# Performance work log

Hardware: AMD Instinct MI355X
Metric: run time of the kernel (lower is better)

Reference implementation:

```python
import jax, jax.numpy as jnp
import numpy as np

D_MODEL = 1024
N = 32  # d_state // 2
L_LEN = 4096


def setup_inputs() -> dict:
    key = jax.random.key(0)
    k1, k2, k3 = jax.random.split(key, 3)
    dt_min, dt_max = 1e-3, 1e-1
    log_dt = jax.random.uniform(k1, (D_MODEL,), dtype=jnp.float32) * (
        np.log(dt_max) - np.log(dt_min)
    ) + np.log(dt_min)
    C_ri = jax.random.normal(k2, (D_MODEL, N, 2), dtype=jnp.float32)
    log_A_real = jnp.log(0.5 * jnp.ones((D_MODEL, N), dtype=jnp.float32))
    A_imag = np.pi * jnp.broadcast_to(
        jnp.arange(N, dtype=jnp.float32)[None, :], (D_MODEL, N)
    )
    return {
        "L": L_LEN,
        "log_dt": log_dt,
        "C_ri": C_ri,
        "log_A_real": log_A_real,
        "A_imag": A_imag,
    }


def reference(L, log_dt, C_ri, log_A_real, A_imag):
    dt = jnp.exp(log_dt)  # (H,)
    C = C_ri[..., 0] + 1j * C_ri[..., 1]  # (H, N) complex
    A = -jnp.exp(log_A_real) + 1j * A_imag  # (H, N)
    dtA = A * dt[:, None]  # (H, N)
    # Vandermonde: exp(dtA * l) for l in [0, L)
    l = jnp.arange(L, dtype=jnp.float32)
    V = jnp.exp(dtA[:, :, None] * l[None, None, :])  # (H, N, L) complex
    Ceff = C * (jnp.exp(dtA) - 1.0) / A  # (H, N)
    K = 2.0 * jnp.einsum("hn,hnl->hl", Ceff, V).real  # (H, L)
    return K
```

## Files before the change

kernel.cpp:

```cpp
#include <hip/hip_runtime.h>


#define HD   1024
#define NS   32
#define LL   4096
#define BLK  256
#define NJ   (LL / BLK)

__global__ __launch_bounds__(BLK) void s4d_kernel(
    const float* __restrict__ log_dt,
    const float* __restrict__ C_ri,
    const float* __restrict__ log_A_real,
    const float* __restrict__ A_imag,
    float* __restrict__ K)
{
    const int h   = blockIdx.x;
    const int tid = threadIdx.x;

    __shared__ float  s_wr[NS], s_wi[NS];
    __shared__ float  s_cr[NS], s_ci[NS];
    __shared__ float  s_a[NS];
    __shared__ double s_b[NS];

    const double TWO_PI     = 6.283185307179586;
    const double INV_TWO_PI = 0.15915494309189535;

    if (tid < NS) {
        const int   n   = tid;
        const float dt  = expf(log_dt[h]);
        const float ar  = -expf(log_A_real[h * NS + n]);
        const float ai  = A_imag[h * NS + n];
        const float a   = ar * dt;
        const double bd = (double)ai * (double)dt;
        const float b   = (float)bd;

        const float e = expf(a);
        float sb, cb;
        sincosf(b, &sb, &cb);
        const float er = fmaf(e, cb, -1.0f);
        const float ei = e * sb;

        const float den = fmaf(ar, ar, ai * ai);
        const float inv = 1.0f / den;
        const float fr  = fmaf(er, ar,  ei * ai) * inv;
        const float fi  = fmaf(ei, ar, -er * ai) * inv;

        const float Cr = C_ri[(h * NS + n) * 2 + 0];
        const float Ci = C_ri[(h * NS + n) * 2 + 1];
        s_cr[n] = 2.0f * fmaf(Cr, fr, -Ci * fi);
        s_ci[n] = 2.0f * fmaf(Cr, fi,  Ci * fr);

        double ph = bd * 256.0;
        ph -= floor(ph * INV_TWO_PI) * TWO_PI;
        float sw, cw;
        sincosf((float)ph, &sw, &cw);
        const float e256 = expf(a * 256.0f);
        s_wr[n] = e256 * cw;
        s_wi[n] = e256 * sw;
        s_a[n]  = a;
        s_b[n]  = bd;
    }
    __syncthreads();

    float acc[NJ];
#pragma unroll
    for (int j = 0; j < NJ; ++j) acc[j] = 0.0f;

    for (int n = 0; n < NS; ++n) {
        const float  a = s_a[n];
        const double b = s_b[n];

        const float mag = expf(a * (float)tid);
        double ph = b * (double)tid;
        ph -= floor(ph * INV_TWO_PI) * TWO_PI;
        float sp, cp;
        sincosf((float)ph, &sp, &cp);
        float zr = mag * cp;
        float zi = mag * sp;

        const float wr = s_wr[n], wi = s_wi[n];
        const float cr = s_cr[n], ci = s_ci[n];

#pragma unroll
        for (int j = 0; j < NJ; ++j) {
            acc[j] = fmaf(cr, zr, fmaf(-ci, zi, acc[j]));
            const float t = fmaf(zr, wr, -zi * wi);
            zi = fmaf(zr, wi, zi * wr);
            zr = t;
        }
    }

    float* out = K + h * LL + tid;
#pragma unroll
    for (int j = 0; j < NJ; ++j) out[j * BLK] = acc[j];
}

extern "C" void kernel_launch(void* const* d_in, const int* in_sizes, int n_in,
                              void* d_out, int out_size, void* d_ws, size_t ws_size,
                              hipStream_t stream) {
    const float* log_dt     = (const float*)d_in[1];
    const float* C_ri       = (const float*)d_in[2];
    const float* log_A_real = (const float*)d_in[3];
    const float* A_imag     = (const float*)d_in[4];
    float* K = (float*)d_out;

    s4d_kernel<<<dim3(HD), dim3(BLK), 0, stream>>>(log_dt, C_ri, log_A_real, A_imag, K);
}
```

Baseline: 94.10 us.

## Use a real second-order recurrence with packed float2 math over paired modes

```diff
diff --git a/kernel.cpp b/kernel.cpp
--- a/kernel.cpp
+++ b/kernel.cpp
@@ -6,6 +6,8 @@
 #define LL   4096
 #define BLK  256
 #define NJ   (LL / BLK)
+
+typedef float v2 __attribute__((ext_vector_type(2)));
 
 __global__ __launch_bounds__(BLK) void s4d_kernel(
     const float* __restrict__ log_dt,
@@ -17,16 +19,19 @@
     const int h   = blockIdx.x;
     const int tid = threadIdx.x;
 
-    __shared__ float  s_wr[NS], s_wi[NS];
-    __shared__ float  s_cr[NS], s_ci[NS];
-    __shared__ float  s_a[NS];
-    __shared__ double s_b[NS];
+    __shared__ v2 s_wr[NS / 2], s_wi[NS / 2];
+    __shared__ v2 s_q[NS / 2];
+    __shared__ v2 s_c2r[NS / 2], s_c2i[NS / 2];
+    __shared__ v2 s_al2[NS / 2];
+    __shared__ double s_rb[NS];
 
     const double TWO_PI     = 6.283185307179586;
     const double INV_TWO_PI = 0.15915494309189535;
+    const float  TWO_PI_F   = 6.2831853f;
 
     if (tid < NS) {
         const int   n   = tid;
+        const int   sl  = ((n & 15) << 1) | (n >> 4);
         const float dt  = expf(log_dt[h]);
         const float ar  = -expf(log_A_real[h * NS + n]);
         const float ai  = A_imag[h * NS + n];
@@ -47,52 +52,71 @@
 
         const float Cr = C_ri[(h * NS + n) * 2 + 0];
         const float Ci = C_ri[(h * NS + n) * 2 + 1];
-        s_cr[n] = 2.0f * fmaf(Cr, fr, -Ci * fi);
-        s_ci[n] = 2.0f * fmaf(Cr, fi,  Ci * fr);
+        ((float*)s_c2r)[sl] = 2.0f * fmaf(Cr, fr, -Ci * fi);
+        ((float*)s_c2i)[sl] = 2.0f * fmaf(Cr, fi,  Ci * fr);
 
         double ph = bd * 256.0;
         ph -= floor(ph * INV_TWO_PI) * TWO_PI;
         float sw, cw;
         sincosf((float)ph, &sw, &cw);
         const float e256 = expf(a * 256.0f);
-        s_wr[n] = e256 * cw;
-        s_wi[n] = e256 * sw;
-        s_a[n]  = a;
-        s_b[n]  = bd;
+        ((float*)s_wr)[sl]  = e256 * cw;
+        ((float*)s_wi)[sl]  = e256 * sw;
+        ((float*)s_q)[sl]   = e256 * e256;
+        ((float*)s_al2)[sl] = a * 1.4426950408889634f;
+        s_rb[n] = bd * INV_TWO_PI;
     }
     __syncthreads();
 
-    float acc[NJ];
+    v2 acc[NJ];
 #pragma unroll
-    for (int j = 0; j < NJ; ++j) acc[j] = 0.0f;
+    for (int j = 0; j < NJ; ++j) acc[j] = (v2)(0.0f);
 
-    for (int n = 0; n < NS; ++n) {
-        const float  a = s_a[n];
-        const double b = s_b[n];
+    const float t = (float)tid;
 
-        const float mag = expf(a * (float)tid);
-        double ph = b * (double)tid;
-        ph -= floor(ph * INV_TWO_PI) * TWO_PI;
-        float sp, cp;
-        sincosf((float)ph, &sp, &cp);
-        float zr = mag * cp;
-        float zi = mag * sp;
+    for (int np = 0; np < NS / 2; ++np) {
+        const v2 al2 = s_al2[np];
+        const v2 wr  = s_wr[np];
+        const v2 wi  = s_wi[np];
+        const v2 q   = s_q[np];
+        const v2 c2r = s_c2r[np];
+        const v2 c2i = s_c2i[np];
 
-        const float wr = s_wr[n], wi = s_wi[n];
-        const float cr = s_cr[n], ci = s_ci[n];
+        v2 mag;
+        mag.x = __builtin_amdgcn_exp2f(al2.x * t);
+        mag.y = __builtin_amdgcn_exp2f(al2.y * t);
 
+        double r0 = s_rb[np] * (double)tid;        r0 -= floor(r0);
+        double r1 = s_rb[np + 16] * (double)tid;   r1 -= floor(r1);
+        const float f0 = (float)r0 * TWO_PI_F;
+        const float f1 = (float)r1 * TWO_PI_F;
+
+        v2 zr, zi;
+        zr.x = mag.x * __cosf(f0);
+        zr.y = mag.y * __cosf(f1);
+        zi.x = mag.x * __sinf(f0);
+        zi.y = mag.y * __sinf(f1);
+
+        v2 u0 = c2r * zr - c2i * zi;
+        v2 zwr = zr * wr - zi * wi;
+        v2 zwi = zr * wi + zi * wr;
+        v2 u1 = c2r * zwr - c2i * zwi;
+        const v2 p = wr + wr;
+
+        acc[0] += u0;
+        acc[1] += u1;
 #pragma unroll
-        for (int j = 0; j < NJ; ++j) {
-            acc[j] = fmaf(cr, zr, fmaf(-ci, zi, acc[j]));
-            const float t = fmaf(zr, wr, -zi * wi);
-            zi = fmaf(zr, wi, zi * wr);
-            zr = t;
+        for (int j = 2; j < NJ; ++j) {
+            const v2 u = p * u1 - q * u0;
+            acc[j] += u;
+            u0 = u1;
+            u1 = u;
         }
     }
 
     float* out = K + h * LL + tid;
 #pragma unroll
-    for (int j = 0; j < NJ; ++j) out[j * BLK] = acc[j];
+    for (int j = 0; j < NJ; ++j) out[j * BLK] = acc[j].x + acc[j].y;
 }
 
 extern "C" void kernel_launch(void* const* d_in, const int* in_sizes, int n_in,
```

Result: faster. 78.96 us (-16.1%).
